# Optimization experiments

Measured on AMD Instinct MI355X. Metric: run time of the kernel, lower is better.

Reference implementation:

```python
import jax, jax.numpy as jnp
import numpy as np

N = 262144            # inflated nodes (atoms + edge-nodes)
E = 4 * 1024 * 1024   # directed edges
D = 8                 # node_feature_dim
TD = 1                # time_dim
H = 32                # hidden_channels
L = 4                 # num_layers
BN_EPS = 1e-5


def setup_inputs() -> dict:
    key = jax.random.key(0)
    ks = jax.random.split(key, 12)
    s = 0.1  # small init scale
    return {
        "x": jax.random.normal(ks[0], (N, D), jnp.float32),
        "t": jax.random.uniform(ks[1], (1,), jnp.float32),
        "edge_index": jax.random.randint(ks[2], (2, E), 0, N, jnp.int32),
        "node_mask": jax.random.randint(ks[3], (N,), 0, 2) > 0,
        "edge_mask": jax.random.randint(ks[4], (N,), 0, 2) > 0,
        "ond": 5,  # original_node_feature_dim
        "oed": 4,  # original_edge_feature_dim
        # GINConv MLP params: layer 0 has in=D+TD, layers 1..3 have in=H
        "W1_first": jax.random.normal(ks[5], (D + TD, H), jnp.float32) * s,
        "b1_first": jnp.zeros((H,), jnp.float32),
        "W2_first": jax.random.normal(ks[6], (H, H), jnp.float32) * s,
        "b2_first": jnp.zeros((H,), jnp.float32),
        "W1_rest": jax.random.normal(ks[7], (L - 1, H, H), jnp.float32) * s,
        "b1_rest": jnp.zeros((L - 1, H), jnp.float32),
        "W2_rest": jax.random.normal(ks[8], (L - 1, H, H), jnp.float32) * s,
        "b2_rest": jnp.zeros((L - 1, H), jnp.float32),
        "eps": jnp.zeros((L,), jnp.float32),           # train_eps=True, init 0
        "bn_gamma": jnp.ones((L, H), jnp.float32),
        "bn_beta": jnp.zeros((L, H), jnp.float32),
        "lin_W": jax.random.normal(ks[9], (L * H, D), jnp.float32) * s,
        "lin_b": jnp.zeros((D,), jnp.float32),
    }


def _gin_forward(x, t, W1_first, b1_first, W2_first, b2_first,
                 W1_rest, b1_rest, W2_rest, b2_rest, eps, bn_gamma, bn_beta,
                 lin_W, lin_b, edge_index, node_mask, edge_mask, ond, oed):
    src = edge_index[0]
    dst = edge_index[1]
    n = x.shape[0]
    # x_in = cat(x, t*ones)
    tcol = jnp.full((n, 1), t[0], x.dtype)
    h = jnp.concatenate([x, tcol], axis=1)  # [N, D+TD]
    xs = []
    for l in range(L):
        # GINConv: (1+eps)*x_i + sum_{j->i} x_j, then 2-layer MLP
        agg = jax.ops.segment_sum(h[src], dst, num_segments=n)  # scatter-add
        z = (1.0 + eps[l]) * h + agg
        W1 = W1_first if l == 0 else W1_rest[l - 1]
        b1 = b1_first if l == 0 else b1_rest[l - 1]
        W2 = W2_first if l == 0 else W2_rest[l - 1]
        b2 = b2_first if l == 0 else b2_rest[l - 1]
        z = jax.nn.relu(z @ W1 + b1) @ W2 + b2  # [N, H]
        # BatchNorm (training-mode batch stats), then ReLU; dropout=eval->id
        mu = jnp.mean(z, axis=0)
        var = jnp.var(z, axis=0)
        z = (z - mu) * jax.lax.rsqrt(var + BN_EPS) * bn_gamma[l] + bn_beta[l]
        h = jax.nn.relu(z)
        xs.append(h)
    # JK 'cat' + final Linear(L*H -> D)
    new_x = jnp.concatenate(xs, axis=1) @ lin_W + lin_b  # [N, D]
    # masked feature write-back: x[mask, 1:dim+1] = new_x[mask, 1:dim+1]
    cols = jnp.arange(x.shape[1])
    ncols = (cols >= 1) & (cols < ond + 1)
    ecols = (cols >= 1) & (cols < oed + 1)
    out = jnp.where(node_mask[:, None] & ncols[None, :], new_x, x)
    out = jnp.where(edge_mask[:, None] & ecols[None, :], new_x, out)
    return out


def reference(x, t, edge_index, node_mask, edge_mask, ond, oed,
              W1_first, b1_first, W2_first, b2_first,
              W1_rest, b1_rest, W2_rest, b2_rest,
              eps, bn_gamma, bn_beta, lin_W, lin_b):
    return _gin_forward(x, t, W1_first, b1_first, W2_first, b2_first,
                        W1_rest, b1_rest, W2_rest, b2_rest,
                        eps, bn_gamma, bn_beta, lin_W, lin_b,
                        edge_index, node_mask, edge_mask, ond, oed)
```

## Files before the change

### kernel.cpp

```cpp
#include <hip/hip_runtime.h>
#include <cstdint>

#define NN 262144
#define EE 4194304
#define CAP 64
#define NB 512
#define BSZ 512
#define NSH 8
#define SCAP 1280
#define EPB 8192
#define SLICES 64

__device__ inline float bf2f(unsigned short u) {
  union { unsigned int i; float f; } v; v.i = ((unsigned int)u) << 16; return v.f;
}
__device__ inline unsigned short f2bf(float f) {
  union { float f; unsigned int i; } v; v.f = f;
  unsigned int r = v.i + 0x7FFF + ((v.i >> 16) & 1);
  return (unsigned short)(r >> 16);
}
__device__ inline float blo(unsigned int u) {
  union { unsigned int i; float f; } v; v.i = u << 16; return v.f;
}
__device__ inline float bhi(unsigned int u) {
  union { unsigned int i; float f; } v; v.i = u & 0xFFFF0000u; return v.f;
}

__global__ void k_curinit(int* __restrict__ cur) {
  int i = blockIdx.x * 256 + threadIdx.x;
  if (i < NSH * NB) cur[i] = i * SCAP;
}

__global__ void __launch_bounds__(256, 1)
k_bin(const int* __restrict__ ei, int* __restrict__ cur, int* __restrict__ pair) {
  __shared__ int hist[NB];
  __shared__ int off[NB];
  __shared__ int gbase[NB];
  __shared__ int psum[256];
  __shared__ int ebuf[EPB];
  const int tid = threadIdx.x, blk = blockIdx.x, sh = blk & (NSH - 1);
  const int* esrc = ei + (size_t)blk * EPB;
  const int* edst = ei + EE + (size_t)blk * EPB;

  for (int k = tid; k < NB; k += 256) hist[k] = 0;
  __syncthreads();
  for (int j = tid; j < EPB / 4; j += 256) {
    int4 d4 = ((const int4*)edst)[j];
    atomicAdd(&hist[d4.x >> 9], 1);
    atomicAdd(&hist[d4.y >> 9], 1);
    atomicAdd(&hist[d4.z >> 9], 1);
    atomicAdd(&hist[d4.w >> 9], 1);
  }
  __syncthreads();
  int a0 = hist[2 * tid], a1 = hist[2 * tid + 1];
  int ps = a0 + a1;
  psum[tid] = ps;
  __syncthreads();
  for (int d = 1; d < 256; d <<= 1) {
    int v = (tid >= d) ? psum[tid - d] : 0;
    __syncthreads();
    psum[tid] += v;
    __syncthreads();
  }
  int excl = psum[tid] - ps;
  off[2 * tid] = excl;
  off[2 * tid + 1] = excl + a0;
  __syncthreads();
  for (int b = tid; b < NB; b += 256) {
    int n = hist[b];
    int ci = sh * NB + b;
    gbase[b] = n ? atomicAdd(&cur[ci], n) : ci * SCAP;
  }
  __syncthreads();
  for (int k = tid; k < NB; k += 256) hist[k] = off[k];
  __syncthreads();
  for (int j = tid; j < EPB / 4; j += 256) {
    int4 s4 = ((const int4*)esrc)[j];
    int4 d4 = ((const int4*)edst)[j];
    int dd[4] = {d4.x, d4.y, d4.z, d4.w};
    int ss[4] = {s4.x, s4.y, s4.z, s4.w};
#pragma unroll
    for (int u = 0; u < 4; ++u) {
      int bin = dd[u] >> 9, dl = dd[u] & (BSZ - 1);
      int p = atomicAdd(&hist[bin], 1);
      ebuf[p] = ss[u] | (dl << 18);
    }
  }
  __syncthreads();
  for (int b = tid; b < NB; b += 256) {
    int st = off[b];
    int n = hist[b] - st;
    int ci = sh * NB + b;
    int gb = gbase[b];
    int lim = ci * SCAP + SCAP;
    if (gb + n > lim) n = (lim > gb) ? (lim - gb) : 0;
    for (int k = 0; k < n; ++k) pair[gb + k] = ebuf[st + k];
  }
}

__global__ void k_expand(const int* __restrict__ cur, const int* __restrict__ pair,
                         int* __restrict__ slot, int* __restrict__ deg) {
  __shared__ int cbin[BSZ];
  int tid = threadIdx.x;
  int bin = blockIdx.x;
  for (int k = tid; k < BSZ; k += 512) cbin[k] = 0;
  __syncthreads();
  for (int s = 0; s < NSH; ++s) {
    int ci = s * NB + bin, base = ci * SCAP;
    int cnt = min(cur[ci] - base, SCAP);
    for (int k = tid; k < cnt; k += 512) {
      int p = pair[base + k];
      int src = p & 0x3FFFF, dl = p >> 18;
      int pos = atomicAdd(&cbin[dl], 1);
      if (pos < CAP)
        slot[((size_t)bin * BSZ + dl) * CAP + pos] = src;
    }
  }
  __syncthreads();
  for (int k = tid; k < BSZ; k += 512) {
    int cnt = min(cbin[k], CAP);
    int cntp = (cnt + 15) & ~15;
    int self = bin * BSZ + k;
    for (int p = cnt; p < cntp; ++p)
      slot[((size_t)bin * BSZ + k) * CAP + p] = self;
    deg[bin * BSZ + k] = cnt;
  }
}

__global__ void k_layer0(const float* __restrict__ x, const float* __restrict__ t,
                         const int* __restrict__ slot, const int* __restrict__ deg,
                         const float* __restrict__ W1, const float* __restrict__ b1,
                         const float* __restrict__ W2, const float* __restrict__ b2,
                         const float* __restrict__ epsv,
                         unsigned short* __restrict__ zb,
                         float* __restrict__ ssum, float* __restrict__ ssq) {
  __shared__ float W1s[9 * 32];
  __shared__ float W2s[32 * 32];
  __shared__ float aggs[8][8];
  __shared__ float ins[8][12];
  __shared__ float z1s[8][36];
  __shared__ float sqs[8][36];
  int tid = threadIdx.x;
  int c = tid & 31, g = tid >> 5;
  size_t i = (size_t)blockIdx.x * 8 + g;

  for (int k = tid; k < 9 * 32 / 4; k += 256) ((float4*)W1s)[k] = ((const float4*)W1)[k];
  for (int k = tid; k < 32 * 32 / 4; k += 256) ((float4*)W2s)[k] = ((const float4*)W2)[k];

  int cnt = deg[i];
  int cntp = (cnt + 15) & ~15;
  const int* sl = slot + i * CAP;
  int sv = sl[c];
  float t0 = t[0];
  float epsl = epsv[0];
  float xself = (c < 8) ? x[i * 8 + c] : 0.f;

  int q = c & 1, e = c >> 1;
  float4 agg4 = {0.f, 0.f, 0.f, 0.f};
  int kmax = min(cntp, 32);
  for (int k = 0; k < kmax; k += 16) {
    int s = __shfl(sv, k + e, 32);
    float4 v = ((const float4*)x)[(size_t)s * 2 + q];
    agg4.x += v.x; agg4.y += v.y; agg4.z += v.z; agg4.w += v.w;
  }
  if (cntp > 32) {
    int sv2 = sl[32 + c];
    for (int k = 32; k < cntp; k += 16) {
      int s = __shfl(sv2, (k - 32) + e, 32);
      float4 v = ((const float4*)x)[(size_t)s * 2 + q];
      agg4.x += v.x; agg4.y += v.y; agg4.z += v.z; agg4.w += v.w;
    }
  }
#pragma unroll
  for (int off = 2; off < 32; off <<= 1) {
    agg4.x += __shfl_xor(agg4.x, off, 32);
    agg4.y += __shfl_xor(agg4.y, off, 32);
    agg4.z += __shfl_xor(agg4.z, off, 32);
    agg4.w += __shfl_xor(agg4.w, off, 32);
  }
  if (c < 2) ((float4*)aggs[g])[q] = agg4;
  __syncthreads();

  float pad = (float)(cntp - cnt);
  if (c < 8)       ins[g][c] = (1.f + epsl) * xself + aggs[g][c] - pad * xself;
  else if (c == 8) ins[g][8] = (1.f + epsl) * t0 + (float)cnt * t0;
  __syncthreads();

  float acc = b1[c];
#pragma unroll
  for (int d = 0; d < 9; ++d) acc += ins[g][d] * W1s[d * 32 + c];
  float z1 = fmaxf(acc, 0.f);
  z1s[g][c] = z1;
  __syncthreads();

  float acc2 = b2[c];
#pragma unroll
  for (int d = 0; d < 32; ++d) acc2 += z1s[g][d] * W2s[d * 32 + c];
  zb[i * 32 + c] = f2bf(acc2);

  __syncthreads();
  z1s[g][c] = acc2;
  sqs[g][c] = acc2 * acc2;
  __syncthreads();
  if (g == 0) {
    float s1 = 0.f, s2 = 0.f;
#pragma unroll
    for (int n = 0; n < 8; ++n) { s1 += z1s[n][c]; s2 += sqs[n][c]; }
    int slice = blockIdx.x & (SLICES - 1);
    atomicAdd(&ssum[slice * 32 + c], s1);
    atomicAdd(&ssq[slice * 32 + c], s2);
  }
}

__global__ void k_bnapply(const unsigned short* __restrict__ zb,
                          const float* __restrict__ ssum, const float* __restrict__ ssq,
                          const float* __restrict__ gamma, const float* __restrict__ beta,
                          const float* __restrict__ linW,
                          unsigned short* __restrict__ hb,
                          float* __restrict__ out_acc, int first_acc) {
  __shared__ float linWs[256];
  __shared__ float scs[32], shs[32];
  int tid = threadIdx.x;
  for (int k = tid; k < 256; k += 256) linWs[k] = linW[k];
  if (tid < 32) {
    float s1 = 0.f, s2 = 0.f;
    for (int s = 0; s < SLICES; ++s) { s1 += ssum[s * 32 + tid]; s2 += ssq[s * 32 + tid]; }
    float mu = s1 * (1.f / NN);
    float var = s2 * (1.f / NN) - mu * mu;
    float sc = gamma[tid] * rsqrtf(var + 1e-5f);
    scs[tid] = sc;
    shs[tid] = beta[tid] - mu * sc;
  }
  int r = tid & 3;
  size_t n = (size_t)blockIdx.x * 64 + (tid >> 2);
  uint4 u = ((const uint4*)zb)[n * 4 + r];
  __syncthreads();

  float h[8];
#pragma unroll
  for (int j = 0; j < 8; ++j) {
    unsigned int w = (j < 2) ? u.x : (j < 4) ? u.y : (j < 6) ? u.z : u.w;
    float zv = (j & 1) ? bhi(w) : blo(w);
    h[j] = fmaxf(zv * scs[8 * r + j] + shs[8 * r + j], 0.f);
  }
  uint4 o;
  o.x = (unsigned int)f2bf(h[0]) | ((unsigned int)f2bf(h[1]) << 16);
  o.y = (unsigned int)f2bf(h[2]) | ((unsigned int)f2bf(h[3]) << 16);
  o.z = (unsigned int)f2bf(h[4]) | ((unsigned int)f2bf(h[5]) << 16);
  o.w = (unsigned int)f2bf(h[6]) | ((unsigned int)f2bf(h[7]) << 16);
  ((uint4*)hb)[n * 4 + r] = o;

  float jk[8];
#pragma unroll
  for (int d = 0; d < 8; ++d) {
    float a = 0.f;
#pragma unroll
    for (int j = 0; j < 8; ++j) a += h[j] * linWs[(8 * r + j) * 8 + d];
    jk[d] = a;
  }
#pragma unroll
  for (int off = 1; off <= 2; off <<= 1)
#pragma unroll
    for (int d = 0; d < 8; ++d) jk[d] += __shfl_xor(jk[d], off, 64);
  if (r == 0) {
    float4 a0 = {jk[0], jk[1], jk[2], jk[3]};
    float4 a1 = {jk[4], jk[5], jk[6], jk[7]};
    if (!first_acc) {
      float4 p0 = ((const float4*)out_acc)[n * 2];
      float4 p1 = ((const float4*)out_acc)[n * 2 + 1];
      a0.x += p0.x; a0.y += p0.y; a0.z += p0.z; a0.w += p0.w;
      a1.x += p1.x; a1.y += p1.y; a1.z += p1.z; a1.w += p1.w;
    }
    ((float4*)out_acc)[n * 2] = a0;
    ((float4*)out_acc)[n * 2 + 1] = a1;
  }
}

__global__ void k_layerN(const unsigned short* __restrict__ hb,
                         const int* __restrict__ slot, const int* __restrict__ deg,
                         const float* __restrict__ W1, const float* __restrict__ b1,
                         const float* __restrict__ W2, const float* __restrict__ b2,
                         const float* __restrict__ epsv, int l,
                         unsigned short* __restrict__ zbo,
                         float* __restrict__ ssum, float* __restrict__ ssq) {
  __shared__ float W1s[32 * 32];
  __shared__ float W2s[32 * 32];
  __shared__ float aggs[8][32];
  __shared__ float ins[8][36];
  __shared__ float z1s[8][36];
  int tid = threadIdx.x;
  int c = tid & 31, g = tid >> 5;
  size_t i = (size_t)blockIdx.x * 8 + g;

  for (int k = tid; k < 32 * 32 / 4; k += 256) {
    ((float4*)W1s)[k] = ((const float4*)W1)[k];
    ((float4*)W2s)[k] = ((const float4*)W2)[k];
  }

  float epsl = epsv[l];
  int cnt = deg[i];
  int cntp = (cnt + 15) & ~15;
  const int* sl = slot + i * CAP;
  int sv = sl[c];
  float hself = bf2f(hb[i * 32 + c]);

  int q = c & 7, sub = c >> 3;
  const ushort4* h4 = (const ushort4*)hb;
  float4 agg4 = {0.f, 0.f, 0.f, 0.f};
  int kmax = min(cntp, 32);
  for (int k = 0; k < kmax; k += 16) {
    int sa = __shfl(sv, k + sub, 32);
    int sb = __shfl(sv, k + 4 + sub, 32);
    int sc_ = __shfl(sv, k + 8 + sub, 32);
    int sd = __shfl(sv, k + 12 + sub, 32);
    ushort4 ua = h4[(size_t)sa * 8 + q];
    ushort4 ub = h4[(size_t)sb * 8 + q];
    ushort4 uc = h4[(size_t)sc_ * 8 + q];
    ushort4 ud = h4[(size_t)sd * 8 + q];
    agg4.x += bf2f(ua.x) + bf2f(ub.x) + bf2f(uc.x) + bf2f(ud.x);
    agg4.y += bf2f(ua.y) + bf2f(ub.y) + bf2f(uc.y) + bf2f(ud.y);
    agg4.z += bf2f(ua.z) + bf2f(ub.z) + bf2f(uc.z) + bf2f(ud.z);
    agg4.w += bf2f(ua.w) + bf2f(ub.w) + bf2f(uc.w) + bf2f(ud.w);
  }
  if (cntp > 32) {
    int sv2 = sl[32 + c];
    for (int k = 32; k < cntp; k += 16) {
      int kk = k - 32;
      int sa = __shfl(sv2, kk + sub, 32);
      int sb = __shfl(sv2, kk + 4 + sub, 32);
      int sc_ = __shfl(sv2, kk + 8 + sub, 32);
      int sd = __shfl(sv2, kk + 12 + sub, 32);
      ushort4 ua = h4[(size_t)sa * 8 + q];
      ushort4 ub = h4[(size_t)sb * 8 + q];
      ushort4 uc = h4[(size_t)sc_ * 8 + q];
      ushort4 ud = h4[(size_t)sd * 8 + q];
      agg4.x += bf2f(ua.x) + bf2f(ub.x) + bf2f(uc.x) + bf2f(ud.x);
      agg4.y += bf2f(ua.y) + bf2f(ub.y) + bf2f(uc.y) + bf2f(ud.y);
      agg4.z += bf2f(ua.z) + bf2f(ub.z) + bf2f(uc.z) + bf2f(ud.z);
      agg4.w += bf2f(ua.w) + bf2f(ub.w) + bf2f(uc.w) + bf2f(ud.w);
    }
  }
  agg4.x += __shfl_xor(agg4.x, 8, 32);
  agg4.y += __shfl_xor(agg4.y, 8, 32);
  agg4.z += __shfl_xor(agg4.z, 8, 32);
  agg4.w += __shfl_xor(agg4.w, 8, 32);
  agg4.x += __shfl_xor(agg4.x, 16, 32);
  agg4.y += __shfl_xor(agg4.y, 16, 32);
  agg4.z += __shfl_xor(agg4.z, 16, 32);
  agg4.w += __shfl_xor(agg4.w, 16, 32);
  if (c < 8) ((float4*)aggs[g])[q] = agg4;
  __syncthreads();

  float pad = (float)(cntp - cnt);
  float inval = (1.f + epsl - pad) * hself + aggs[g][c];
  ins[g][c] = inval;
  __syncthreads();

  float acc = b1[c];
#pragma unroll
  for (int d = 0; d < 32; ++d) acc += ins[g][d] * W1s[d * 32 + c];
  float z1 = fmaxf(acc, 0.f);
  z1s[g][c] = z1;
  __syncthreads();

  float acc2 = b2[c];
#pragma unroll
  for (int d = 0; d < 32; ++d) acc2 += z1s[g][d] * W2s[d * 32 + c];
  zbo[i * 32 + c] = f2bf(acc2);

  __syncthreads();
  ins[g][c] = acc2;
  z1s[g][c] = acc2 * acc2;
  __syncthreads();
  if (g == 0) {
    float s1 = 0.f, s2 = 0.f;
#pragma unroll
    for (int n = 0; n < 8; ++n) { s1 += ins[n][c]; s2 += z1s[n][c]; }
    int slice = blockIdx.x & (SLICES - 1);
    atomicAdd(&ssum[slice * 32 + c], s1);
    atomicAdd(&ssq[slice * 32 + c], s2);
  }
}

__global__ void k_final(const unsigned short* __restrict__ z3,
                        const float* __restrict__ ssum, const float* __restrict__ ssq,
                        const float* __restrict__ gamma, const float* __restrict__ beta,
                        const float* __restrict__ linW3, const float* __restrict__ lin_b,
                        const float* __restrict__ out_acc, const float* __restrict__ x,
                        const int* __restrict__ nm, const int* __restrict__ em,
                        const int* __restrict__ ondp, const int* __restrict__ oedp,
                        float* __restrict__ out) {
  __shared__ float linWs[256];
  __shared__ float scs[32], shs[32];
  int tid = threadIdx.x;
  for (int k = tid; k < 256; k += 256) linWs[k] = linW3[k];
  if (tid < 32) {
    float s1 = 0.f, s2 = 0.f;
    for (int s = 0; s < SLICES; ++s) { s1 += ssum[s * 32 + tid]; s2 += ssq[s * 32 + tid]; }
    float mu = s1 * (1.f / NN);
    float var = s2 * (1.f / NN) - mu * mu;
    float sc = gamma[tid] * rsqrtf(var + 1e-5f);
    scs[tid] = sc;
    shs[tid] = beta[tid] - mu * sc;
  }
  int r = tid & 3;
  size_t n = (size_t)blockIdx.x * 64 + (tid >> 2);
  uint4 u = ((const uint4*)z3)[n * 4 + r];
  __syncthreads();

  float h[8];
#pragma unroll
  for (int j = 0; j < 8; ++j) {
    unsigned int w = (j < 2) ? u.x : (j < 4) ? u.y : (j < 6) ? u.z : u.w;
    float zv = (j & 1) ? bhi(w) : blo(w);
    h[j] = fmaxf(zv * scs[8 * r + j] + shs[8 * r + j], 0.f);
  }
  float jk[8];
#pragma unroll
  for (int d = 0; d < 8; ++d) {
    float a = 0.f;
#pragma unroll
    for (int j = 0; j < 8; ++j) a += h[j] * linWs[(8 * r + j) * 8 + d];
    jk[d] = a;
  }
#pragma unroll
  for (int off = 1; off <= 2; off <<= 1)
#pragma unroll
    for (int d = 0; d < 8; ++d) jk[d] += __shfl_xor(jk[d], off, 64);
  if (r == 0) {
    float4 p0 = ((const float4*)out_acc)[n * 2];
    float4 p1 = ((const float4*)out_acc)[n * 2 + 1];
    float4 x0 = ((const float4*)x)[n * 2];
    float4 x1 = ((const float4*)x)[n * 2 + 1];
    float res[8] = {jk[0] + p0.x + lin_b[0], jk[1] + p0.y + lin_b[1],
                    jk[2] + p0.z + lin_b[2], jk[3] + p0.w + lin_b[3],
                    jk[4] + p1.x + lin_b[4], jk[5] + p1.y + lin_b[5],
                    jk[6] + p1.z + lin_b[6], jk[7] + p1.w + lin_b[7]};
    float xs[8] = {x0.x, x0.y, x0.z, x0.w, x1.x, x1.y, x1.z, x1.w};
    int ond = ondp[0], oed = oedp[0];
    bool nmv = nm[n] != 0, emv = em[n] != 0;
    float o[8];
#pragma unroll
    for (int d = 0; d < 8; ++d) {
      bool w = (d >= 1) && ((nmv && d < ond + 1) || (emv && d < oed + 1));
      o[d] = w ? res[d] : xs[d];
    }
    ((float4*)out)[n * 2]     = make_float4(o[0], o[1], o[2], o[3]);
    ((float4*)out)[n * 2 + 1] = make_float4(o[4], o[5], o[6], o[7]);
  }
}

extern "C" void kernel_launch(void* const* d_in, const int* in_sizes, int n_in,
                              void* d_out, int out_size, void* d_ws, size_t ws_size,
                              hipStream_t stream) {
  const float* x        = (const float*)d_in[0];
  const float* t        = (const float*)d_in[1];
  const int*   ei       = (const int*)d_in[2];
  const int*   node_mask= (const int*)d_in[3];
  const int*   edge_mask= (const int*)d_in[4];
  const int*   ondp     = (const int*)d_in[5];
  const int*   oedp     = (const int*)d_in[6];
  const float* W1_first = (const float*)d_in[7];
  const float* b1_first = (const float*)d_in[8];
  const float* W2_first = (const float*)d_in[9];
  const float* b2_first = (const float*)d_in[10];
  const float* W1_rest  = (const float*)d_in[11];
  const float* b1_rest  = (const float*)d_in[12];
  const float* W2_rest  = (const float*)d_in[13];
  const float* b2_rest  = (const float*)d_in[14];
  const float* epsv     = (const float*)d_in[15];
  const float* bn_gamma = (const float*)d_in[16];
  const float* bn_beta  = (const float*)d_in[17];
  const float* lin_W    = (const float*)d_in[18];
  const float* lin_b    = (const float*)d_in[19];
  float* out = (float*)d_out;

  char* ws = (char*)d_ws;
  size_t off = 0;
  int*   slot    = (int*)(ws + off);   off += (size_t)NN * CAP * 4;
  int*   pair    = (int*)(ws + off);   off += (size_t)NSH * NB * SCAP * 4;
  int*   cur     = (int*)(ws + off);   off += (size_t)NSH * NB * 4;
  int*   deg     = (int*)(ws + off);   off += (size_t)NN * 4;
  unsigned short* zb = (unsigned short*)(ws + off); off += (size_t)NN * 32 * 2;
  unsigned short* hb = (unsigned short*)(ws + off); off += (size_t)NN * 32 * 2;
  float* out_acc = (float*)(ws + off); off += (size_t)NN * 8 * 4;
  float* stats   = (float*)(ws + off); off += (size_t)4 * 2 * SLICES * 32 * 4;
  (void)ws_size; (void)in_sizes; (void)n_in; (void)out_size;

  hipMemsetAsync(stats, 0, (size_t)4 * 2 * SLICES * 32 * 4, stream);
  k_curinit<<<(NSH * NB + 255) / 256, 256, 0, stream>>>(cur);
  k_bin<<<EE / EPB, 256, 0, stream>>>(ei, cur, pair);
  k_expand<<<NB, 512, 0, stream>>>(cur, pair, slot, deg);

  {
    float* ssum = stats;
    float* ssq  = ssum + SLICES * 32;
    k_layer0<<<NN / 8, 256, 0, stream>>>(x, t, slot, deg, W1_first, b1_first,
                                         W2_first, b2_first, epsv, zb, ssum, ssq);
    k_bnapply<<<NN / 64, 256, 0, stream>>>(zb, ssum, ssq, bn_gamma, bn_beta,
                                           lin_W, hb, out_acc, 1);
  }
  for (int l = 1; l < 4; ++l) {
    const float* W1 = W1_rest + (size_t)(l - 1) * 32 * 32;
    const float* b1 = b1_rest + (size_t)(l - 1) * 32;
    const float* W2 = W2_rest + (size_t)(l - 1) * 32 * 32;
    const float* b2 = b2_rest + (size_t)(l - 1) * 32;
    float* ssum = stats + (size_t)l * 2 * SLICES * 32;
    float* ssq  = ssum + SLICES * 32;
    k_layerN<<<NN / 8, 256, 0, stream>>>(hb, slot, deg, W1, b1, W2, b2,
                                         epsv, l, zb, ssum, ssq);
    if (l < 3)
      k_bnapply<<<NN / 64, 256, 0, stream>>>(zb, ssum, ssq, bn_gamma + l * 32,
                                             bn_beta + l * 32,
                                             lin_W + (size_t)l * 32 * 8,
                                             hb, out_acc, 0);
  }
  k_final<<<NN / 64, 256, 0, stream>>>(zb, stats + 3 * 2 * SLICES * 32,
                                       stats + 3 * 2 * SLICES * 32 + SLICES * 32,
                                       bn_gamma + 96, bn_beta + 96,
                                       lin_W + 3 * 32 * 8, lin_b, out_acc, x,
                                       node_mask, edge_mask, ondp, oedp, out);
}
```

Measured before the change: 579.3 us.

## Merge init launches, widen binning blocks, transpose MLP weights for vector LDS reads

Drops the cursor-init kernel by making the cursors relative counts and zeroing them together with the BN stats in a single memset, which needs the workspace reordered so both are contiguous. The binning kernel now runs 512 threads per block, one thread per bin, so the scan and bin loops lose their strided iterations. The layer kernels store W1 and W2 transposed and padded in shared memory so each output channel's dot product reads float4 vectors instead of 32 scalar loads. The intent is fewer launches and fewer LDS instructions, at the cost of an uncoalesced strided transposed load of the weights in every block.

```diff
diff --git a/kernel.cpp b/kernel.cpp
--- a/kernel.cpp
+++ b/kernel.cpp
@@ -26,25 +26,20 @@
   union { unsigned int i; float f; } v; v.i = u & 0xFFFF0000u; return v.f;
 }
 
-__global__ void k_curinit(int* __restrict__ cur) {
-  int i = blockIdx.x * 256 + threadIdx.x;
-  if (i < NSH * NB) cur[i] = i * SCAP;
-}
-
-__global__ void __launch_bounds__(256, 1)
+__global__ void __launch_bounds__(512, 1)
 k_bin(const int* __restrict__ ei, int* __restrict__ cur, int* __restrict__ pair) {
   __shared__ int hist[NB];
   __shared__ int off[NB];
   __shared__ int gbase[NB];
-  __shared__ int psum[256];
+  __shared__ int psum[NB];
   __shared__ int ebuf[EPB];
   const int tid = threadIdx.x, blk = blockIdx.x, sh = blk & (NSH - 1);
   const int* esrc = ei + (size_t)blk * EPB;
   const int* edst = ei + EE + (size_t)blk * EPB;
 
-  for (int k = tid; k < NB; k += 256) hist[k] = 0;
-  __syncthreads();
-  for (int j = tid; j < EPB / 4; j += 256) {
+  if (tid < NB) hist[tid] = 0;
+  __syncthreads();
+  for (int j = tid; j < EPB / 4; j += 512) {
     int4 d4 = ((const int4*)edst)[j];
     atomicAdd(&hist[d4.x >> 9], 1);
     atomicAdd(&hist[d4.y >> 9], 1);
@@ -52,29 +47,27 @@
     atomicAdd(&hist[d4.w >> 9], 1);
   }
   __syncthreads();
-  int a0 = hist[2 * tid], a1 = hist[2 * tid + 1];
-  int ps = a0 + a1;
+  int ps = hist[tid];
   psum[tid] = ps;
   __syncthreads();
-  for (int d = 1; d < 256; d <<= 1) {
+  for (int d = 1; d < NB; d <<= 1) {
     int v = (tid >= d) ? psum[tid - d] : 0;
     __syncthreads();
     psum[tid] += v;
     __syncthreads();
   }
   int excl = psum[tid] - ps;
-  off[2 * tid] = excl;
-  off[2 * tid + 1] = excl + a0;
-  __syncthreads();
-  for (int b = tid; b < NB; b += 256) {
-    int n = hist[b];
-    int ci = sh * NB + b;
-    gbase[b] = n ? atomicAdd(&cur[ci], n) : ci * SCAP;
-  }
-  __syncthreads();
-  for (int k = tid; k < NB; k += 256) hist[k] = off[k];
-  __syncthreads();
-  for (int j = tid; j < EPB / 4; j += 256) {
+  off[tid] = excl;
+  {
+    int n = ps;
+    int ci = sh * NB + tid;
+    int rel = n ? atomicAdd(&cur[ci], n) : 0;
+    gbase[tid] = ci * SCAP + rel;
+  }
+  __syncthreads();
+  hist[tid] = excl;
+  __syncthreads();
+  for (int j = tid; j < EPB / 4; j += 512) {
     int4 s4 = ((const int4*)esrc)[j];
     int4 d4 = ((const int4*)edst)[j];
     int dd[4] = {d4.x, d4.y, d4.z, d4.w};
@@ -87,11 +80,11 @@
     }
   }
   __syncthreads();
-  for (int b = tid; b < NB; b += 256) {
-    int st = off[b];
-    int n = hist[b] - st;
-    int ci = sh * NB + b;
-    int gb = gbase[b];
+  {
+    int st = off[tid];
+    int n = hist[tid] - st;
+    int ci = sh * NB + tid;
+    int gb = gbase[tid];
     int lim = ci * SCAP + SCAP;
     if (gb + n > lim) n = (lim > gb) ? (lim - gb) : 0;
     for (int k = 0; k < n; ++k) pair[gb + k] = ebuf[st + k];
@@ -107,7 +100,7 @@
   __syncthreads();
   for (int s = 0; s < NSH; ++s) {
     int ci = s * NB + bin, base = ci * SCAP;
-    int cnt = min(cur[ci] - base, SCAP);
+    int cnt = min(cur[ci], SCAP);
     for (int k = tid; k < cnt; k += 512) {
       int p = pair[base + k];
       int src = p & 0x3FFFF, dl = p >> 18;
@@ -134,8 +127,8 @@
                          const float* __restrict__ epsv,
                          unsigned short* __restrict__ zb,
                          float* __restrict__ ssum, float* __restrict__ ssq) {
-  __shared__ float W1s[9 * 32];
-  __shared__ float W2s[32 * 32];
+  __shared__ float W1t[32 * 12];
+  __shared__ float W2t[32 * 36];
   __shared__ float aggs[8][8];
   __shared__ float ins[8][12];
   __shared__ float z1s[8][36];
@@ -144,8 +137,14 @@
   int c = tid & 31, g = tid >> 5;
   size_t i = (size_t)blockIdx.x * 8 + g;
 
-  for (int k = tid; k < 9 * 32 / 4; k += 256) ((float4*)W1s)[k] = ((const float4*)W1)[k];
-  for (int k = tid; k < 32 * 32 / 4; k += 256) ((float4*)W2s)[k] = ((const float4*)W2)[k];
+  for (int k = tid; k < 32 * 12; k += 256) {
+    int cc = k / 12, dd = k % 12;
+    W1t[k] = (dd < 9) ? W1[dd * 32 + cc] : 0.f;
+  }
+  for (int k = tid; k < 32 * 32; k += 256) {
+    int dd = k >> 5, cc = k & 31;
+    W2t[cc * 36 + dd] = W2[k];
+  }
 
   int cnt = deg[i];
   int cntp = (cnt + 15) & ~15;
@@ -184,18 +183,35 @@
   float pad = (float)(cntp - cnt);
   if (c < 8)       ins[g][c] = (1.f + epsl) * xself + aggs[g][c] - pad * xself;
   else if (c == 8) ins[g][8] = (1.f + epsl) * t0 + (float)cnt * t0;
+  else if (c < 12) ins[g][c] = 0.f;
   __syncthreads();
 
   float acc = b1[c];
-#pragma unroll
-  for (int d = 0; d < 9; ++d) acc += ins[g][d] * W1s[d * 32 + c];
+  {
+    const float4* iv4 = (const float4*)&ins[g][0];
+    const float4* wv4 = (const float4*)&W1t[c * 12];
+#pragma unroll
+    for (int dd = 0; dd < 3; ++dd) {
+      float4 iv = iv4[dd];
+      float4 wv = wv4[dd];
+      acc += iv.x * wv.x + iv.y * wv.y + iv.z * wv.z + iv.w * wv.w;
+    }
+  }
   float z1 = fmaxf(acc, 0.f);
   z1s[g][c] = z1;
   __syncthreads();
 
   float acc2 = b2[c];
-#pragma unroll
-  for (int d = 0; d < 32; ++d) acc2 += z1s[g][d] * W2s[d * 32 + c];
+  {
+    const float4* iv4 = (const float4*)&z1s[g][0];
+    const float4* wv4 = (const float4*)&W2t[c * 36];
+#pragma unroll
+    for (int dd = 0; dd < 8; ++dd) {
+      float4 iv = iv4[dd];
+      float4 wv = wv4[dd];
+      acc2 += iv.x * wv.x + iv.y * wv.y + iv.z * wv.z + iv.w * wv.w;
+    }
+  }
   zb[i * 32 + c] = f2bf(acc2);
 
   __syncthreads();
@@ -283,8 +299,8 @@
                          const float* __restrict__ epsv, int l,
                          unsigned short* __restrict__ zbo,
                          float* __restrict__ ssum, float* __restrict__ ssq) {
-  __shared__ float W1s[32 * 32];
-  __shared__ float W2s[32 * 32];
+  __shared__ float W1t[32 * 36];
+  __shared__ float W2t[32 * 36];
   __shared__ float aggs[8][32];
   __shared__ float ins[8][36];
   __shared__ float z1s[8][36];
@@ -292,9 +308,10 @@
   int c = tid & 31, g = tid >> 5;
   size_t i = (size_t)blockIdx.x * 8 + g;
 
-  for (int k = tid; k < 32 * 32 / 4; k += 256) {
-    ((float4*)W1s)[k] = ((const float4*)W1)[k];
-    ((float4*)W2s)[k] = ((const float4*)W2)[k];
+  for (int k = tid; k < 32 * 32; k += 256) {
+    int dd = k >> 5, cc = k & 31;
+    W1t[cc * 36 + dd] = W1[k];
+    W2t[cc * 36 + dd] = W2[k];
   }
 
   float epsl = epsv[l];
@@ -357,15 +374,31 @@
   __syncthreads();
 
   float acc = b1[c];
-#pragma unroll
-  for (int d = 0; d < 32; ++d) acc += ins[g][d] * W1s[d * 32 + c];
+  {
+    const float4* iv4 = (const float4*)&ins[g][0];
+    const float4* wv4 = (const float4*)&W1t[c * 36];
+#pragma unroll
+    for (int dd = 0; dd < 8; ++dd) {
+      float4 iv = iv4[dd];
+      float4 wv = wv4[dd];
+      acc += iv.x * wv.x + iv.y * wv.y + iv.z * wv.z + iv.w * wv.w;
+    }
+  }
   float z1 = fmaxf(acc, 0.f);
   z1s[g][c] = z1;
   __syncthreads();
 
   float acc2 = b2[c];
-#pragma unroll
-  for (int d = 0; d < 32; ++d) acc2 += z1s[g][d] * W2s[d * 32 + c];
+  {
+    const float4* iv4 = (const float4*)&z1s[g][0];
+    const float4* wv4 = (const float4*)&W2t[c * 36];
+#pragma unroll
+    for (int dd = 0; dd < 8; ++dd) {
+      float4 iv = iv4[dd];
+      float4 wv = wv4[dd];
+      acc2 += iv.x * wv.x + iv.y * wv.y + iv.z * wv.z + iv.w * wv.w;
+    }
+  }
   zbo[i * 32 + c] = f2bf(acc2);
 
   __syncthreads();
@@ -480,16 +513,16 @@
   int*   slot    = (int*)(ws + off);   off += (size_t)NN * CAP * 4;
   int*   pair    = (int*)(ws + off);   off += (size_t)NSH * NB * SCAP * 4;
   int*   cur     = (int*)(ws + off);   off += (size_t)NSH * NB * 4;
+  float* stats   = (float*)(ws + off); off += (size_t)4 * 2 * SLICES * 32 * 4;
   int*   deg     = (int*)(ws + off);   off += (size_t)NN * 4;
   unsigned short* zb = (unsigned short*)(ws + off); off += (size_t)NN * 32 * 2;
   unsigned short* hb = (unsigned short*)(ws + off); off += (size_t)NN * 32 * 2;
   float* out_acc = (float*)(ws + off); off += (size_t)NN * 8 * 4;
-  float* stats   = (float*)(ws + off); off += (size_t)4 * 2 * SLICES * 32 * 4;
   (void)ws_size; (void)in_sizes; (void)n_in; (void)out_size;
 
-  hipMemsetAsync(stats, 0, (size_t)4 * 2 * SLICES * 32 * 4, stream);
-  k_curinit<<<(NSH * NB + 255) / 256, 256, 0, stream>>>(cur);
-  k_bin<<<EE / EPB, 256, 0, stream>>>(ei, cur, pair);
+  hipMemsetAsync(cur, 0, (size_t)NSH * NB * 4 + (size_t)4 * 2 * SLICES * 32 * 4,
+                 stream);
+  k_bin<<<EE / EPB, 512, 0, stream>>>(ei, cur, pair);
   k_expand<<<NB, 512, 0, stream>>>(cur, pair, slot, deg);
 
   {
```

Result: slower. 598.9 us (+3.4%).
